# Performance work log

Hardware: AMD Instinct MI355X
Metric: run time of the kernel (lower is better)

## Reference

```python
import jax, jax.numpy as jnp
import numpy as np

B, T_Q, T_KV, D = 4, 2048, 4096, 1024
H = 16
HD = D // H  # head_dim = 64
EPS_LN = 1e-5
EPS_NORM = 1e-12


def setup_inputs() -> dict:
    key = jax.random.key(0)
    ks = jax.random.split(key, 12)
    inp = {
        'query': jax.random.normal(ks[0], (B, T_Q, D), jnp.float32),
        'key':   jax.random.normal(ks[1], (B, T_KV, D), jnp.float32),
        'value': jax.random.normal(ks[2], (B, T_KV, D), jnp.float32),
        # projections (nn.Linear stores weight as [out, in]; y = x @ W.T)
        'Wq': jax.random.normal(ks[3], (D, D), jnp.float32) * 0.02,
        'Wk': jax.random.normal(ks[4], (D, D), jnp.float32) * 0.02,
        'Wv': jax.random.normal(ks[5], (D, D), jnp.float32) * 0.02,
        'Wo': jax.random.normal(ks[6], (D, D), jnp.float32) * 0.01,
        'bo': jnp.zeros((D,), jnp.float32),
        'Wbeta':  jax.random.normal(ks[7], (H, D), jnp.float32) * 0.02,
        'bbeta':  jnp.zeros((H,), jnp.float32),
        'Walpha': jax.random.normal(ks[8], (H, D), jnp.float32) * 0.02,
        'balpha': jnp.full((H,), -1.0, jnp.float32),
        # per-head-dim LayerNorms
        'gq': jnp.ones((HD,), jnp.float32),
        'bq': jnp.zeros((HD,), jnp.float32),
        'gk': jnp.ones((HD,), jnp.float32),
        'bk': jnp.zeros((HD,), jnp.float32),
    }
    return inp


def _layernorm(x, g, b):
    mu = jnp.mean(x, axis=-1, keepdims=True)
    var = jnp.mean(jnp.square(x - mu), axis=-1, keepdims=True)
    return (x - mu) * jax.lax.rsqrt(var + EPS_LN) * g + b


def reference(query, key, value, Wq, Wk, Wv, Wo, bo,
              Wbeta, bbeta, Walpha, balpha, gq, bq, gk, bk):
    Bq, Tq, Dm = query.shape
    Tkv = key.shape[1]

    q = (query @ Wq.T).reshape(Bq, Tq, H, HD)
    k = (key   @ Wk.T).reshape(Bq, Tkv, H, HD)
    v = (value @ Wv.T).reshape(Bq, Tkv, H, HD)

    q = _layernorm(q, gq, bq)
    k = _layernorm(k, gk, bk)
    # F.normalize(k, dim=-1)
    k = k / jnp.maximum(jnp.linalg.norm(k, axis=-1, keepdims=True), EPS_NORM)

    beta  = jax.nn.sigmoid(key @ Wbeta.T  + bbeta)   # [B, Tkv, H]
    alpha = jax.nn.sigmoid(key @ Walpha.T + balpha)  # [B, Tkv, H]

    # time-major for scan: [Tkv, B, H, ...]
    k_t = jnp.moveaxis(k, 1, 0)
    v_t = jnp.moveaxis(v, 1, 0)
    b_t = jnp.moveaxis(beta, 1, 0)
    a_t = jnp.moveaxis(alpha, 1, 0)

    M0 = jnp.zeros((Bq, H, HD, HD), query.dtype)

    def step(M, inputs):
        kt, vt, bt, at = inputs  # [B,H,d],[B,H,d],[B,H],[B,H]
        Mk = jnp.einsum('bhij,bhj->bhi', M, kt)
        erase = at[..., None, None] * jnp.einsum('bhi,bhj->bhij', Mk, kt)
        write = bt[..., None, None] * jnp.einsum('bhi,bhj->bhij', vt, kt)
        return M - erase + write, None

    M, _ = jax.lax.scan(step, M0, (k_t, v_t, b_t, a_t))

    # out[b,t,h,i] = sum_j M[b,h,i,j] * q[b,t,h,j]
    out = jnp.einsum('bhij,bthj->bthi', M, q).reshape(Bq, Tq, Dm)
    out = out @ Wo.T + bo  # dropout is identity in eval mode
    return out
```

## Files before the change

kernel.cpp:

```cpp
#include <hip/hip_runtime.h>
#include <math.h>

#define TQ_LEN 2048
#define TKV_LEN 4096
#define BATCH 4
#define DMODEL 1024
#define NH 16
#define HD 64
#define NKBA 1280
#define CCH 128
#define NCHUNK (TKV_LEN / CCH)

typedef unsigned short u16;
typedef __attribute__((ext_vector_type(8))) short bf16x8;
typedef __attribute__((ext_vector_type(4))) float f32x4;

__device__ __forceinline__ u16 f2bf(float x) {
  union { float f; unsigned u; } c; c.f = x;
  unsigned r = c.u + 0x7fffu + ((c.u >> 16) & 1u);
  return (u16)(r >> 16);
}
__device__ __forceinline__ float bf2f(u16 x) {
  union { unsigned u; float f; } c; c.u = ((unsigned)x) << 16;
  return c.f;
}

__device__ __forceinline__ float wave_sum64(float x) {
#pragma unroll
  for (int off = 32; off; off >>= 1) x += __shfl_xor(x, off, 64);
  return x;
}

__global__ __launch_bounds__(256) void cvt_bf16_kernel(
    const float* __restrict__ s, u16* __restrict__ d) {
  size_t i = ((size_t)blockIdx.x * 256 + threadIdx.x) * 8;
  float4 a = *(const float4*)&s[i];
  float4 b = *(const float4*)&s[i + 4];
  union { u16 h[8]; uint4 v; } o;
  o.h[0] = f2bf(a.x); o.h[1] = f2bf(a.y); o.h[2] = f2bf(a.z); o.h[3] = f2bf(a.w);
  o.h[4] = f2bf(b.x); o.h[5] = f2bf(b.y); o.h[6] = f2bf(b.z); o.h[7] = f2bf(b.w);
  *(uint4*)&d[i] = o.v;
}

__global__ __launch_bounds__(256) void wcat_bf_kernel(
    const float* __restrict__ Wk, const float* __restrict__ Wb,
    const float* __restrict__ Wa, u16* __restrict__ Wcat) {
  int i = blockIdx.x * 256 + threadIdx.x;
  int row = i / DMODEL, col = i % DMODEL;
  float v;
  if (row < 1024)      v = Wk[i];
  else if (row < 1040) v = Wb[(row - 1024) * DMODEL + col];
  else if (row < 1056) v = Wa[(row - 1040) * DMODEL + col];
  else                 v = 0.f;
  Wcat[i] = f2bf(v);
}

#define BAR() __builtin_amdgcn_s_barrier()
#define PRIO(x) __builtin_amdgcn_s_setprio(x)
#define VMCNT(n)                                              \
  do {                                                        \
    __builtin_amdgcn_sched_barrier(0);                        \
    asm volatile("s_waitcnt vmcnt(" #n ")" ::: "memory");     \
  } while (0)

__device__ __forceinline__ void stage_half256(
    const u16* __restrict__ G, int ldg, int row0, int kc, int h,
    u16* ldsmat, int wid, int lane) {
#pragma unroll
  for (int e = 0; e < 2; ++e) {
    int j0 = wid * 64 + e * 512;
    int j = j0 + lane;
    int r = h * 128 + (j >> 3);
    int cg = (j & 7) * 8;
    const u16* g = G + (size_t)(row0 + r) * ldg + kc + cg;
    __builtin_amdgcn_global_load_lds(
        (const __attribute__((address_space(1))) void*)g,
        (__attribute__((address_space(3))) void*)(ldsmat + h * 8192 + j0 * 8),
        16, 0, 0);
  }
}

#define READ_A(L, h_)                                                         \
  do {                                                                        \
    _Pragma("unroll") for (int mf = 0; mf < 4; ++mf)                          \
    _Pragma("unroll") for (int kk = 0; kk < 2; ++kk)                          \
      af[mf][kk] = *(const bf16x8*)&(L)[(wm * 128 + (h_) * 64 + mf * 16 +     \
                                         lrow) * 64 + kk * 32 + lk8];         \
  } while (0)

#define READ_B(L, n_, dst)                                                    \
  do {                                                                        \
    _Pragma("unroll") for (int nf = 0; nf < 2; ++nf)                          \
    _Pragma("unroll") for (int kk = 0; kk < 2; ++kk)                          \
      dst[nf][kk] = *(const bf16x8*)&(L)[(wn * 64 + (n_) * 32 + nf * 16 +     \
                                          lrow) * 64 + kk * 32 + lk8];        \
  } while (0)

#define MFMA_Q(h_, n_, bfx)                                                   \
  do {                                                                        \
    _Pragma("unroll") for (int mf = 0; mf < 4; ++mf)                          \
    _Pragma("unroll") for (int nf = 0; nf < 2; ++nf)                          \
    _Pragma("unroll") for (int kk = 0; kk < 2; ++kk)                          \
      acc[h_][mf][n_][nf] = __builtin_amdgcn_mfma_f32_16x16x32_bf16(          \
          af[mf][kk], bfx[nf][kk], acc[h_][mf][n_][nf], 0, 0, 0);             \
  } while (0)

template <bool HAS_BIAS, bool OUT_BF16>
__global__ __launch_bounds__(512, 2) void gemm_bt_256(
    const u16* __restrict__ A, const u16* __restrict__ B,
    const float* __restrict__ bias, void* __restrict__ Cv,
    int K, int ldc, int nbx) {
  __shared__ u16 lds[2][2][16384];
  const int tid = threadIdx.x;
  const int lane = tid & 63, wid = tid >> 6;
  const int wm = wid >> 2, wn = wid & 3;
  const int nwg = gridDim.x, cpx = nwg >> 3, orig = blockIdx.x;
  const int swz = (orig & 7) * cpx + (orig >> 3);
  const int bm = (swz / nbx) * 256, bn = (swz % nbx) * 256;
  const int lrow = lane & 15, lk8 = (lane >> 4) * 8;
  const int NT = K >> 6;

  f32x4 acc[2][4][2][2] = {};
  bf16x8 af[4][2], bf0[2][2], bf1[2][2];

  u16* lA0 = &lds[0][0][0]; u16* lB0 = &lds[0][1][0];
  u16* lA1 = &lds[1][0][0]; u16* lB1 = &lds[1][1][0];

  stage_half256(A, K, bm, 0, 0, lA0, wid, lane);
  stage_half256(A, K, bm, 0, 1, lA0, wid, lane);
  stage_half256(B, K, bn, 0, 0, lB0, wid, lane);
  stage_half256(B, K, bn, 0, 1, lB0, wid, lane);
  stage_half256(B, K, bn, 64, 0, lB1, wid, lane);
  stage_half256(B, K, bn, 64, 1, lB1, wid, lane);
  VMCNT(0);
  BAR();

  for (int i = 0; i < NT / 2; ++i) {
    const int t0 = 2 * i, t1 = 2 * i + 1;
    READ_A(lA0, 0);
    READ_B(lB0, 0, bf0);
    stage_half256(A, K, bm, t1 * 64, 0, lA1, wid, lane);
    BAR(); PRIO(1); MFMA_Q(0, 0, bf0); PRIO(0); BAR();
    READ_B(lB0, 1, bf1);
    stage_half256(A, K, bm, t1 * 64, 1, lA1, wid, lane);
    BAR(); PRIO(1); MFMA_Q(0, 1, bf1); PRIO(0); BAR();
    READ_A(lA0, 1);
    if (t0 + 2 < NT) stage_half256(B, K, bn, (t0 + 2) * 64, 0, lB0, wid, lane);
    BAR(); PRIO(1); MFMA_Q(1, 0, bf0); PRIO(0); BAR();
    if (t0 + 2 < NT) stage_half256(B, K, bn, (t0 + 2) * 64, 1, lB0, wid, lane);
    BAR(); PRIO(1); MFMA_Q(1, 1, bf1); PRIO(0);
    VMCNT(4);
    BAR();
    READ_A(lA1, 0);
    READ_B(lB1, 0, bf0);
    if (t0 + 2 < NT) stage_half256(A, K, bm, (t0 + 2) * 64, 0, lA0, wid, lane);
    BAR(); PRIO(1); MFMA_Q(0, 0, bf0); PRIO(0); BAR();
    READ_B(lB1, 1, bf1);
    if (t0 + 2 < NT) stage_half256(A, K, bm, (t0 + 2) * 64, 1, lA0, wid, lane);
    BAR(); PRIO(1); MFMA_Q(0, 1, bf1); PRIO(0); BAR();
    READ_A(lA1, 1);
    if (t1 + 2 < NT) stage_half256(B, K, bn, (t1 + 2) * 64, 0, lB1, wid, lane);
    BAR(); PRIO(1); MFMA_Q(1, 0, bf0); PRIO(0); BAR();
    if (t1 + 2 < NT) stage_half256(B, K, bn, (t1 + 2) * 64, 1, lB1, wid, lane);
    BAR(); PRIO(1); MFMA_Q(1, 1, bf1); PRIO(0);
    VMCNT(4);
    BAR();
  }

#pragma unroll
  for (int h = 0; h < 2; ++h)
#pragma unroll
    for (int n = 0; n < 2; ++n)
#pragma unroll
      for (int mf = 0; mf < 4; ++mf)
#pragma unroll
        for (int nf = 0; nf < 2; ++nf) {
          int col = bn + wn * 64 + n * 32 + nf * 16 + (lane & 15);
          float bv = HAS_BIAS ? bias[col] : 0.f;
          int row0 = bm + wm * 128 + h * 64 + mf * 16 + (lane >> 4) * 4;
#pragma unroll
          for (int ii = 0; ii < 4; ++ii) {
            float vout = acc[h][mf][n][nf][ii] + bv;
            if (OUT_BF16)
              ((u16*)Cv)[(size_t)(row0 + ii) * ldc + col] = f2bf(vout);
            else
              ((float*)Cv)[(size_t)(row0 + ii) * ldc + col] = vout;
          }
        }
}

__global__ __launch_bounds__(256) void ln_q_kernel(float* __restrict__ q,
                                                   const float* __restrict__ g,
                                                   const float* __restrict__ b) {
  int gidx = blockIdx.x * 4 + (threadIdx.x >> 6);
  int lane = threadIdx.x & 63;
  int row = gidx >> 4, h = gidx & 15;
  float* p = q + (size_t)row * DMODEL + h * HD + lane;
  float x = *p;
  float mu = wave_sum64(x) * (1.f / 64.f);
  float d = x - mu;
  float var = wave_sum64(d * d) * (1.f / 64.f);
  float y = d * rsqrtf(var + 1e-5f) * g[lane] + b[lane];
  *p = y;
}

__global__ __launch_bounds__(256) void ln_k_kernel(float* __restrict__ kb,
                                                   const float* __restrict__ g,
                                                   const float* __restrict__ b) {
  int gidx = blockIdx.x * 4 + (threadIdx.x >> 6);
  int lane = threadIdx.x & 63;
  int row = gidx >> 4, h = gidx & 15;
  float* p = kb + (size_t)row * NKBA + h * HD + lane;
  float x = *p;
  float mu = wave_sum64(x) * (1.f / 64.f);
  float d = x - mu;
  float var = wave_sum64(d * d) * (1.f / 64.f);
  float y = d * rsqrtf(var + 1e-5f) * g[lane] + b[lane];
  float s2 = wave_sum64(y * y);
  y = y / fmaxf(sqrtf(s2), 1e-12f);
  *p = y;
}

__global__ __launch_bounds__(256) void sig_kernel(
    const float* __restrict__ kb, const float* __restrict__ bb,
    const float* __restrict__ ba, float* __restrict__ beta,
    float* __restrict__ alpha) {
  int i = blockIdx.x * 256 + threadIdx.x;
  int row = i >> 4, h = i & 15;
  float lb = kb[(size_t)row * NKBA + 1024 + h] + bb[h];
  float la = kb[(size_t)row * NKBA + 1040 + h] + ba[h];
  beta[i]  = 1.f / (1.f + expf(-lb));
  alpha[i] = 1.f / (1.f + expf(-la));
}

__global__ __launch_bounds__(64, 2) void chunk_scan_kernel(
    const float* __restrict__ kb, const u16* __restrict__ v,
    const float* __restrict__ beta, const float* __restrict__ alpha,
    float* __restrict__ Pbuf, float* __restrict__ Sbuf) {
  __shared__ float klds[2][64];
  int slot = blockIdx.x;
  int bh = slot / NCHUNK, ck = slot % NCHUNK;
  int b = bh >> 4, h = bh & 15;
  int lane = threadIdx.x;
  int t0 = ck * CCH;
  const float* kbase = kb + ((size_t)b * TKV_LEN + t0) * NKBA + h * HD;
  const u16* vbase = v + ((size_t)b * TKV_LEN + t0) * DMODEL + h * HD;
  const float* bbase = beta + ((size_t)b * TKV_LEN + t0) * NH + h;
  const float* abase = alpha + ((size_t)b * TKV_LEN + t0) * NH + h;

  float P[64], S[64];
#pragma unroll
  for (int j = 0; j < 64; ++j) { P[j] = (j == lane) ? 1.f : 0.f; S[j] = 0.f; }

  klds[0][lane] = kbase[lane];
  float kn = kbase[(size_t)NKBA + lane];
  float vn = bf2f(vbase[lane]);
  float btn = bbase[0];
  float atn = abase[0];

  for (int t = 0; t < CCH; ++t) {
    float vc = vn, bt = btn, at = atn;
    if (t + 1 < CCH) {
      vn = bf2f(vbase[(size_t)(t + 1) * DMODEL + lane]);
      btn = bbase[(size_t)(t + 1) * NH];
      atn = abase[(size_t)(t + 1) * NH];
    }
    klds[(t + 1) & 1][lane] = kn;
    kn = (t + 2 < CCH) ? kbase[(size_t)(t + 2) * NKBA + lane] : 0.f;
    const float* kcur = klds[t & 1];
    float pk0 = 0.f, pk1 = 0.f, sk0 = 0.f, sk1 = 0.f;
#pragma unroll
    for (int g = 0; g < 4; ++g) {
      float4 ka = *(const float4*)&kcur[g * 16 + 0];
      float4 kc = *(const float4*)&kcur[g * 16 + 4];
      float4 ke = *(const float4*)&kcur[g * 16 + 8];
      float4 kg = *(const float4*)&kcur[g * 16 + 12];
      pk0 = fmaf(P[g*16+ 0], ka.x, pk0); pk1 = fmaf(P[g*16+ 1], ka.y, pk1);
      pk0 = fmaf(P[g*16+ 2], ka.z, pk0); pk1 = fmaf(P[g*16+ 3], ka.w, pk1);
      pk0 = fmaf(P[g*16+ 4], kc.x, pk0); pk1 = fmaf(P[g*16+ 5], kc.y, pk1);
      pk0 = fmaf(P[g*16+ 6], kc.z, pk0); pk1 = fmaf(P[g*16+ 7], kc.w, pk1);
      pk0 = fmaf(P[g*16+ 8], ke.x, pk0); pk1 = fmaf(P[g*16+ 9], ke.y, pk1);
      pk0 = fmaf(P[g*16+10], ke.z, pk0); pk1 = fmaf(P[g*16+11], ke.w, pk1);
      pk0 = fmaf(P[g*16+12], kg.x, pk0); pk1 = fmaf(P[g*16+13], kg.y, pk1);
      pk0 = fmaf(P[g*16+14], kg.z, pk0); pk1 = fmaf(P[g*16+15], kg.w, pk1);
      sk0 = fmaf(S[g*16+ 0], ka.x, sk0); sk1 = fmaf(S[g*16+ 1], ka.y, sk1);
      sk0 = fmaf(S[g*16+ 2], ka.z, sk0); sk1 = fmaf(S[g*16+ 3], ka.w, sk1);
      sk0 = fmaf(S[g*16+ 4], kc.x, sk0); sk1 = fmaf(S[g*16+ 5], kc.y, sk1);
      sk0 = fmaf(S[g*16+ 6], kc.z, sk0); sk1 = fmaf(S[g*16+ 7], kc.w, sk1);
      sk0 = fmaf(S[g*16+ 8], ke.x, sk0); sk1 = fmaf(S[g*16+ 9], ke.y, sk1);
      sk0 = fmaf(S[g*16+10], ke.z, sk0); sk1 = fmaf(S[g*16+11], ke.w, sk1);
      sk0 = fmaf(S[g*16+12], kg.x, sk0); sk1 = fmaf(S[g*16+13], kg.y, sk1);
      sk0 = fmaf(S[g*16+14], kg.z, sk0); sk1 = fmaf(S[g*16+15], kg.w, sk1);
    }
    float cp = -at * (pk0 + pk1);
    float cs = fmaf(bt, vc, -at * (sk0 + sk1));
#pragma unroll
    for (int g = 0; g < 4; ++g) {
      float4 ka = *(const float4*)&kcur[g * 16 + 0];
      float4 kc = *(const float4*)&kcur[g * 16 + 4];
      float4 ke = *(const float4*)&kcur[g * 16 + 8];
      float4 kg = *(const float4*)&kcur[g * 16 + 12];
      P[g*16+ 0] = fmaf(cp, ka.x, P[g*16+ 0]); P[g*16+ 1] = fmaf(cp, ka.y, P[g*16+ 1]);
      P[g*16+ 2] = fmaf(cp, ka.z, P[g*16+ 2]); P[g*16+ 3] = fmaf(cp, ka.w, P[g*16+ 3]);
      P[g*16+ 4] = fmaf(cp, kc.x, P[g*16+ 4]); P[g*16+ 5] = fmaf(cp, kc.y, P[g*16+ 5]);
      P[g*16+ 6] = fmaf(cp, kc.z, P[g*16+ 6]); P[g*16+ 7] = fmaf(cp, kc.w, P[g*16+ 7]);
      P[g*16+ 8] = fmaf(cp, ke.x, P[g*16+ 8]); P[g*16+ 9] = fmaf(cp, ke.y, P[g*16+ 9]);
      P[g*16+10] = fmaf(cp, ke.z, P[g*16+10]); P[g*16+11] = fmaf(cp, ke.w, P[g*16+11]);
      P[g*16+12] = fmaf(cp, kg.x, P[g*16+12]); P[g*16+13] = fmaf(cp, kg.y, P[g*16+13]);
      P[g*16+14] = fmaf(cp, kg.z, P[g*16+14]); P[g*16+15] = fmaf(cp, kg.w, P[g*16+15]);
      S[g*16+ 0] = fmaf(cs, ka.x, S[g*16+ 0]); S[g*16+ 1] = fmaf(cs, ka.y, S[g*16+ 1]);
      S[g*16+ 2] = fmaf(cs, ka.z, S[g*16+ 2]); S[g*16+ 3] = fmaf(cs, ka.w, S[g*16+ 3]);
      S[g*16+ 4] = fmaf(cs, kc.x, S[g*16+ 4]); S[g*16+ 5] = fmaf(cs, kc.y, S[g*16+ 5]);
      S[g*16+ 6] = fmaf(cs, kc.z, S[g*16+ 6]); S[g*16+ 7] = fmaf(cs, kc.w, S[g*16+ 7]);
      S[g*16+ 8] = fmaf(cs, ke.x, S[g*16+ 8]); S[g*16+ 9] = fmaf(cs, ke.y, S[g*16+ 9]);
      S[g*16+10] = fmaf(cs, ke.z, S[g*16+10]); S[g*16+11] = fmaf(cs, ke.w, S[g*16+11]);
      S[g*16+12] = fmaf(cs, kg.x, S[g*16+12]); S[g*16+13] = fmaf(cs, kg.y, S[g*16+13]);
      S[g*16+14] = fmaf(cs, kg.z, S[g*16+14]); S[g*16+15] = fmaf(cs, kg.w, S[g*16+15]);
    }
  }
  float* po = Pbuf + (size_t)slot * 4096 + (size_t)lane * 64;
  float* so = Sbuf + (size_t)slot * 4096 + (size_t)lane * 64;
#pragma unroll
  for (int j4 = 0; j4 < 16; ++j4) {
    *(float4*)&po[j4 * 4] = make_float4(P[4 * j4], P[4 * j4 + 1], P[4 * j4 + 2], P[4 * j4 + 3]);
    *(float4*)&so[j4 * 4] = make_float4(S[4 * j4], S[4 * j4 + 1], S[4 * j4 + 2], S[4 * j4 + 3]);
  }
}

__global__ __launch_bounds__(256) void fold_kernel(
    const float* __restrict__ Pin, const float* __restrict__ Sin,
    float* __restrict__ Pout, float* __restrict__ Sout, int nitems) {
  __shared__ float Pa[64][68], Sa[64][68], Pc[64][68], Sc[64][68];
  const int tid = threadIdx.x;
  const int r0 = (tid >> 4) * 4, c0 = (tid & 15) * 4;
  for (int l = tid; l < 4096; l += 256) {
    int r = l >> 6, c = l & 63;
    Pa[r][c] = (r == c) ? 1.f : 0.f;
    Sa[r][c] = 0.f;
  }
  for (int item = 0; item < nitems; ++item) {
    const float* pg = Pin + ((size_t)blockIdx.x * nitems + item) * 4096;
    const float* sg = Sin + ((size_t)blockIdx.x * nitems + item) * 4096;
#pragma unroll
    for (int e = 0; e < 4; ++e) {
      int l = tid * 16 + e * 4;
      int r = l >> 6, c = l & 63;
      *(float4*)&Pc[r][c] = *(const float4*)&pg[l];
      *(float4*)&Sc[r][c] = *(const float4*)&sg[l];
    }
    __syncthreads();
    float accP[4][4] = {}, accS[4][4] = {};
#pragma unroll 4
    for (int j4 = 0; j4 < 16; ++j4) {
      float bmat[4][4];
#pragma unroll
      for (int jj = 0; jj < 4; ++jj) {
        float4 t = *(const float4*)&Pc[j4 * 4 + jj][c0];
        bmat[jj][0] = t.x; bmat[jj][1] = t.y; bmat[jj][2] = t.z; bmat[jj][3] = t.w;
      }
#pragma unroll
      for (int rr = 0; rr < 4; ++rr) {
        float4 tp = *(const float4*)&Pa[r0 + rr][j4 * 4];
        float4 ts = *(const float4*)&Sa[r0 + rr][j4 * 4];
        float ap[4] = {tp.x, tp.y, tp.z, tp.w};
        float as[4] = {ts.x, ts.y, ts.z, ts.w};
#pragma unroll
        for (int jj = 0; jj < 4; ++jj)
#pragma unroll
          for (int cc = 0; cc < 4; ++cc) {
            accP[rr][cc] = fmaf(ap[jj], bmat[jj][cc], accP[rr][cc]);
            accS[rr][cc] = fmaf(as[jj], bmat[jj][cc], accS[rr][cc]);
          }
      }
    }
#pragma unroll
    for (int rr = 0; rr < 4; ++rr)
#pragma unroll
      for (int cc = 0; cc < 4; ++cc) accS[rr][cc] += Sc[r0 + rr][c0 + cc];
    __syncthreads();
#pragma unroll
    for (int rr = 0; rr < 4; ++rr)
#pragma unroll
      for (int cc = 0; cc < 4; ++cc) {
        Pa[r0 + rr][c0 + cc] = accP[rr][cc];
        Sa[r0 + rr][c0 + cc] = accS[rr][cc];
      }
  }
  __syncthreads();
  float* po = Pout + (size_t)blockIdx.x * 4096;
  float* so = Sout + (size_t)blockIdx.x * 4096;
#pragma unroll
  for (int e = 0; e < 4; ++e) {
    int l = tid * 16 + e * 4;
    int r = l >> 6, c = l & 63;
    *(float4*)&po[l] = *(const float4*)&Pa[r][c];
    *(float4*)&so[l] = *(const float4*)&Sa[r][c];
  }
}

__global__ __launch_bounds__(256) void outm_kernel(
    const float* __restrict__ Mg, const float* __restrict__ q,
    u16* __restrict__ attn) {
  __shared__ float Ml[64][65];
  int bh = blockIdx.x;
  int tchunk = blockIdx.y;
  int b = bh >> 4, h = bh & 15;
  int tid = threadIdx.x;
  const float* mg = Mg + (size_t)bh * 4096;
#pragma unroll
  for (int e = 0; e < 16; ++e) {
    int l = tid + e * 256;
    Ml[l >> 6][l & 63] = mg[l];
  }
  __syncthreads();
  int lane = tid & 63, tt = tid >> 6;
  const float* qb = q + ((size_t)b * TQ_LEN + tchunk * 256) * DMODEL + h * HD;
  u16* ob = attn + ((size_t)b * TQ_LEN + tchunk * 256) * DMODEL + h * HD;
  for (int it = 0; it < 64; ++it) {
    int t = it * 4 + tt;
    const float* qr = qb + (size_t)t * DMODEL;
    float acc = 0.f;
#pragma unroll
    for (int j4 = 0; j4 < 16; ++j4) {
      float4 qv = *(const float4*)&qr[j4 * 4];
      acc += Ml[lane][j4 * 4 + 0] * qv.x + Ml[lane][j4 * 4 + 1] * qv.y +
             Ml[lane][j4 * 4 + 2] * qv.z + Ml[lane][j4 * 4 + 3] * qv.w;
    }
    ob[(size_t)t * DMODEL + lane] = f2bf(acc);
  }
}

extern "C" void kernel_launch(void* const* d_in, const int* in_sizes, int n_in,
                              void* d_out, int out_size, void* d_ws,
                              size_t ws_size, hipStream_t stream) {
  const float* query = (const float*)d_in[0];
  const float* key   = (const float*)d_in[1];
  const float* value = (const float*)d_in[2];
  const float* Wq    = (const float*)d_in[3];
  const float* Wk    = (const float*)d_in[4];
  const float* Wv    = (const float*)d_in[5];
  const float* Wo    = (const float*)d_in[6];
  const float* bo    = (const float*)d_in[7];
  const float* Wbeta = (const float*)d_in[8];
  const float* bbeta = (const float*)d_in[9];
  const float* Walpha= (const float*)d_in[10];
  const float* balpha= (const float*)d_in[11];
  const float* gq    = (const float*)d_in[12];
  const float* bq    = (const float*)d_in[13];
  const float* gk    = (const float*)d_in[14];
  const float* bk    = (const float*)d_in[15];
  float* out = (float*)d_out;

  const int MQ = BATCH * TQ_LEN;
  const int MKV = BATCH * TKV_LEN;
  const int NSLOT = 64 * NCHUNK;

  float* ws = (float*)d_ws;
  size_t off = 0;
  u16* Wcat_bf = (u16*)(ws + off); off += (size_t)NKBA * DMODEL / 2;
  u16* Wq_bf   = (u16*)(ws + off); off += (size_t)DMODEL * DMODEL / 2;
  u16* Wv_bf   = (u16*)(ws + off); off += (size_t)DMODEL * DMODEL / 2;
  u16* Wo_bf   = (u16*)(ws + off); off += (size_t)DMODEL * DMODEL / 2;
  u16* qbf = (u16*)(ws + off); size_t qbf_f = off; off += (size_t)MQ * DMODEL / 2;
  u16* kbf = (u16*)(ws + off); size_t kbf_f = off; off += (size_t)MKV * DMODEL / 2;
  u16* vbf = (u16*)(ws + off); size_t vbf_f = off; off += (size_t)MKV * DMODEL / 2;
  float* qp   = ws + off; off += (size_t)MQ * DMODEL;
  float* kba  = ws + off; size_t kba_f = off; off += (size_t)MKV * NKBA;
  u16* vpb = (u16*)(ws + off); off += (size_t)MKV * DMODEL / 2;
  float* Pbuf = ws + kbf_f;
  float* Sbuf = ws + vbf_f;
  float* Gp   = ws + qbf_f;
  float* Gs   = ws + qbf_f + 1048576;
  float* Fp   = ws + qbf_f + 2097152;
  float* beta = ws + qbf_f + 2359296;
  float* alpha= ws + qbf_f + 2621440;
  float* Mg   = ws + qbf_f + 2883584;
  u16* attn_bf = (u16*)(ws + kba_f);

  wcat_bf_kernel<<<NKBA * DMODEL / 256, 256, 0, stream>>>(Wk, Wbeta, Walpha, Wcat_bf);
  cvt_bf16_kernel<<<DMODEL * DMODEL / 2048, 256, 0, stream>>>(Wq, Wq_bf);
  cvt_bf16_kernel<<<DMODEL * DMODEL / 2048, 256, 0, stream>>>(Wv, Wv_bf);
  cvt_bf16_kernel<<<DMODEL * DMODEL / 2048, 256, 0, stream>>>(Wo, Wo_bf);
  cvt_bf16_kernel<<<MQ * DMODEL / 2048, 256, 0, stream>>>(query, qbf);
  cvt_bf16_kernel<<<MKV * DMODEL / 2048, 256, 0, stream>>>(key, kbf);
  cvt_bf16_kernel<<<MKV * DMODEL / 2048, 256, 0, stream>>>(value, vbf);
  gemm_bt_256<false, false><<<(DMODEL / 256) * (MQ / 256), 512, 0, stream>>>(
      qbf, Wq_bf, nullptr, qp, DMODEL, DMODEL, DMODEL / 256);
  gemm_bt_256<false, false><<<(NKBA / 256) * (MKV / 256), 512, 0, stream>>>(
      kbf, Wcat_bf, nullptr, kba, DMODEL, NKBA, NKBA / 256);
  gemm_bt_256<false, true><<<(DMODEL / 256) * (MKV / 256), 512, 0, stream>>>(
      vbf, Wv_bf, nullptr, vpb, DMODEL, DMODEL, DMODEL / 256);
  ln_q_kernel<<<MQ * NH / 4, 256, 0, stream>>>(qp, gq, bq);
  ln_k_kernel<<<MKV * NH / 4, 256, 0, stream>>>(kba, gk, bk);
  sig_kernel<<<MKV * NH / 256, 256, 0, stream>>>(kba, bbeta, balpha, beta, alpha);
  chunk_scan_kernel<<<NSLOT, 64, 0, stream>>>(kba, vpb, beta, alpha, Pbuf, Sbuf);
  fold_kernel<<<NSLOT / 8, 256, 0, stream>>>(Pbuf, Sbuf, Gp, Gs, 8);
  fold_kernel<<<64, 256, 0, stream>>>(Gp, Gs, Fp, Mg, 4);
  outm_kernel<<<dim3(64, TQ_LEN / 256), 256, 0, stream>>>(Mg, qp, attn_bf);
  gemm_bt_256<true, false><<<(DMODEL / 256) * (MQ / 256), 512, 0, stream>>>(
      attn_bf, Wo_bf, bo, out, DMODEL, DMODEL, DMODEL / 256);
  (void)in_sizes; (void)n_in; (void)out_size; (void)ws_size;
}
```

Baseline: 632.9 us.

## Shrink GEMM tiles to 128x256 with XOR-swizzled LDS and restructured pipeline

Replaces the 256x256 bf16 GEMM tile with a 128x256 tile. This halves the accumulator registers and doubles the workgroup count, so more of the CUs are filled for these matrix sizes. It adds an XOR swizzle on the LDS column groups to avoid bank conflicts on the MFMA fragment reads. The load/compute schedule is rewritten with new vmcnt/lgkmcnt waits and barriers. The trade-off is less data reuse per tile (more global traffic for B) and a more intricate wait schedule that could stall or race.

```diff
diff --git a/kernel.cpp b/kernel.cpp
--- a/kernel.cpp
+++ b/kernel.cpp
@@ -62,30 +62,35 @@
     __builtin_amdgcn_sched_barrier(0);                        \
     asm volatile("s_waitcnt vmcnt(" #n ")" ::: "memory");     \
   } while (0)
-
-__device__ __forceinline__ void stage_half256(
-    const u16* __restrict__ G, int ldg, int row0, int kc, int h,
-    u16* ldsmat, int wid, int lane) {
+#define LGKM0()                                               \
+  do {                                                        \
+    asm volatile("s_waitcnt lgkmcnt(0)" ::: "memory");        \
+    __builtin_amdgcn_sched_barrier(0);                        \
+  } while (0)
+
+__device__ __forceinline__ void stage128(
+    const u16* __restrict__ G, int ldg, int row0, int kc,
+    u16* ldsbase, int wid, int lane) {
 #pragma unroll
   for (int e = 0; e < 2; ++e) {
     int j0 = wid * 64 + e * 512;
     int j = j0 + lane;
-    int r = h * 128 + (j >> 3);
-    int cg = (j & 7) * 8;
+    int r = j >> 3;
+    int cg = ((j & 7) ^ (r & 7)) * 8;
     const u16* g = G + (size_t)(row0 + r) * ldg + kc + cg;
     __builtin_amdgcn_global_load_lds(
         (const __attribute__((address_space(1))) void*)g,
-        (__attribute__((address_space(3))) void*)(ldsmat + h * 8192 + j0 * 8),
+        (__attribute__((address_space(3))) void*)(ldsbase + (size_t)j0 * 8),
         16, 0, 0);
   }
 }
 
-#define READ_A(L, h_)                                                         \
+#define READ_A(L)                                                             \
   do {                                                                        \
     _Pragma("unroll") for (int mf = 0; mf < 4; ++mf)                          \
     _Pragma("unroll") for (int kk = 0; kk < 2; ++kk)                          \
-      af[mf][kk] = *(const bf16x8*)&(L)[(wm * 128 + (h_) * 64 + mf * 16 +     \
-                                         lrow) * 64 + kk * 32 + lk8];         \
+      af[mf][kk] = *(const bf16x8*)&(L)[(wm * 64 + mf * 16 + lrow) * 64 +     \
+                                        (((kk * 4 + (lane >> 4)) ^ xorg) * 8)];\
   } while (0)
 
 #define READ_B(L, n_, dst)                                                    \
@@ -93,100 +98,98 @@
     _Pragma("unroll") for (int nf = 0; nf < 2; ++nf)                          \
     _Pragma("unroll") for (int kk = 0; kk < 2; ++kk)                          \
       dst[nf][kk] = *(const bf16x8*)&(L)[(wn * 64 + (n_) * 32 + nf * 16 +     \
-                                          lrow) * 64 + kk * 32 + lk8];        \
+                                          lrow) * 64 +                        \
+                                         (((kk * 4 + (lane >> 4)) ^ xorg) * 8)];\
   } while (0)
 
-#define MFMA_Q(h_, n_, bfx)                                                   \
+#define MFMA_Q(n_, bfx)                                                       \
   do {                                                                        \
     _Pragma("unroll") for (int mf = 0; mf < 4; ++mf)                          \
     _Pragma("unroll") for (int nf = 0; nf < 2; ++nf)                          \
     _Pragma("unroll") for (int kk = 0; kk < 2; ++kk)                          \
-      acc[h_][mf][n_][nf] = __builtin_amdgcn_mfma_f32_16x16x32_bf16(          \
-          af[mf][kk], bfx[nf][kk], acc[h_][mf][n_][nf], 0, 0, 0);             \
+      acc[mf][n_][nf] = __builtin_amdgcn_mfma_f32_16x16x32_bf16(              \
+          af[mf][kk], bfx[nf][kk], acc[mf][n_][nf], 0, 0, 0);                 \
   } while (0)
 
 template <bool HAS_BIAS, bool OUT_BF16>
-__global__ __launch_bounds__(512, 2) void gemm_bt_256(
+__global__ __launch_bounds__(512, 2) void gemm_bt_128x256(
     const u16* __restrict__ A, const u16* __restrict__ B,
     const float* __restrict__ bias, void* __restrict__ Cv,
     int K, int ldc, int nbx) {
-  __shared__ u16 lds[2][2][16384];
+  __shared__ u16 lA[2][8192];
+  __shared__ u16 lB[2][16384];
   const int tid = threadIdx.x;
   const int lane = tid & 63, wid = tid >> 6;
   const int wm = wid >> 2, wn = wid & 3;
   const int nwg = gridDim.x, cpx = nwg >> 3, orig = blockIdx.x;
   const int swz = (orig & 7) * cpx + (orig >> 3);
-  const int bm = (swz / nbx) * 256, bn = (swz % nbx) * 256;
-  const int lrow = lane & 15, lk8 = (lane >> 4) * 8;
+  const int bm = (swz / nbx) * 128, bn = (swz % nbx) * 256;
+  const int lrow = lane & 15;
+  const int xorg = lrow & 7;
   const int NT = K >> 6;
 
-  f32x4 acc[2][4][2][2] = {};
+  f32x4 acc[4][2][2] = {};
   bf16x8 af[4][2], bf0[2][2], bf1[2][2];
 
-  u16* lA0 = &lds[0][0][0]; u16* lB0 = &lds[0][1][0];
-  u16* lA1 = &lds[1][0][0]; u16* lB1 = &lds[1][1][0];
-
-  stage_half256(A, K, bm, 0, 0, lA0, wid, lane);
-  stage_half256(A, K, bm, 0, 1, lA0, wid, lane);
-  stage_half256(B, K, bn, 0, 0, lB0, wid, lane);
-  stage_half256(B, K, bn, 0, 1, lB0, wid, lane);
-  stage_half256(B, K, bn, 64, 0, lB1, wid, lane);
-  stage_half256(B, K, bn, 64, 1, lB1, wid, lane);
+  u16* lA0 = &lA[0][0]; u16* lA1 = &lA[1][0];
+  u16* lB0 = &lB[0][0]; u16* lB1 = &lB[1][0];
+
+  stage128(A, K, bm, 0, lA0, wid, lane);
+  stage128(B, K, bn, 0, lB0, wid, lane);
+  stage128(B, K, bn + 128, 0, lB0 + 8192, wid, lane);
+  stage128(A, K, bm, 64, lA1, wid, lane);
+  stage128(B, K, bn, 64, lB1, wid, lane);
+  stage128(B, K, bn + 128, 64, lB1 + 8192, wid, lane);
   VMCNT(0);
   BAR();
 
   for (int i = 0; i < NT / 2; ++i) {
-    const int t0 = 2 * i, t1 = 2 * i + 1;
-    READ_A(lA0, 0);
+    const int t0 = 2 * i;
+    const bool more = (t0 + 2) < NT;
+    READ_A(lA0);
     READ_B(lB0, 0, bf0);
-    stage_half256(A, K, bm, t1 * 64, 0, lA1, wid, lane);
-    BAR(); PRIO(1); MFMA_Q(0, 0, bf0); PRIO(0); BAR();
     READ_B(lB0, 1, bf1);
-    stage_half256(A, K, bm, t1 * 64, 1, lA1, wid, lane);
-    BAR(); PRIO(1); MFMA_Q(0, 1, bf1); PRIO(0); BAR();
-    READ_A(lA0, 1);
-    if (t0 + 2 < NT) stage_half256(B, K, bn, (t0 + 2) * 64, 0, lB0, wid, lane);
-    BAR(); PRIO(1); MFMA_Q(1, 0, bf0); PRIO(0); BAR();
-    if (t0 + 2 < NT) stage_half256(B, K, bn, (t0 + 2) * 64, 1, lB0, wid, lane);
-    BAR(); PRIO(1); MFMA_Q(1, 1, bf1); PRIO(0);
-    VMCNT(4);
+    BAR(); PRIO(1); MFMA_Q(0, bf0); PRIO(0); BAR();
+    if (more) stage128(A, K, bm, (t0 + 2) * 64, lA0, wid, lane);
+    BAR(); PRIO(1); MFMA_Q(1, bf1); PRIO(0);
+    if (more) { VMCNT(2); } else { VMCNT(0); }
     BAR();
-    READ_A(lA1, 0);
+    READ_A(lA1);
     READ_B(lB1, 0, bf0);
-    if (t0 + 2 < NT) stage_half256(A, K, bm, (t0 + 2) * 64, 0, lA0, wid, lane);
-    BAR(); PRIO(1); MFMA_Q(0, 0, bf0); PRIO(0); BAR();
     READ_B(lB1, 1, bf1);
-    if (t0 + 2 < NT) stage_half256(A, K, bm, (t0 + 2) * 64, 1, lA0, wid, lane);
-    BAR(); PRIO(1); MFMA_Q(0, 1, bf1); PRIO(0); BAR();
-    READ_A(lA1, 1);
-    if (t1 + 2 < NT) stage_half256(B, K, bn, (t1 + 2) * 64, 0, lB1, wid, lane);
-    BAR(); PRIO(1); MFMA_Q(1, 0, bf0); PRIO(0); BAR();
-    if (t1 + 2 < NT) stage_half256(B, K, bn, (t1 + 2) * 64, 1, lB1, wid, lane);
-    BAR(); PRIO(1); MFMA_Q(1, 1, bf1); PRIO(0);
-    VMCNT(4);
+    if (more) stage128(B, K, bn, (t0 + 2) * 64, lB0, wid, lane);
+    BAR(); PRIO(1); MFMA_Q(0, bf0); PRIO(0);
+    LGKM0();
     BAR();
-  }
-
-#pragma unroll
-  for (int h = 0; h < 2; ++h)
-#pragma unroll
-    for (int n = 0; n < 2; ++n)
-#pragma unroll
-      for (int mf = 0; mf < 4; ++mf)
-#pragma unroll
-        for (int nf = 0; nf < 2; ++nf) {
-          int col = bn + wn * 64 + n * 32 + nf * 16 + (lane & 15);
-          float bv = HAS_BIAS ? bias[col] : 0.f;
-          int row0 = bm + wm * 128 + h * 64 + mf * 16 + (lane >> 4) * 4;
-#pragma unroll
-          for (int ii = 0; ii < 4; ++ii) {
-            float vout = acc[h][mf][n][nf][ii] + bv;
-            if (OUT_BF16)
-              ((u16*)Cv)[(size_t)(row0 + ii) * ldc + col] = f2bf(vout);
-            else
-              ((float*)Cv)[(size_t)(row0 + ii) * ldc + col] = vout;
-          }
+    if (more) {
+      stage128(B, K, bn + 128, (t0 + 2) * 64, lB0 + 8192, wid, lane);
+      stage128(A, K, bm, (t0 + 3) * 64, lA1, wid, lane);
+      stage128(B, K, bn, (t0 + 3) * 64, lB1, wid, lane);
+      stage128(B, K, bn + 128, (t0 + 3) * 64, lB1 + 8192, wid, lane);
+    }
+    BAR(); PRIO(1); MFMA_Q(1, bf1); PRIO(0);
+    VMCNT(6);
+    BAR();
+  }
+
+#pragma unroll
+  for (int n = 0; n < 2; ++n)
+#pragma unroll
+    for (int mf = 0; mf < 4; ++mf)
+#pragma unroll
+      for (int nf = 0; nf < 2; ++nf) {
+        int col = bn + wn * 64 + n * 32 + nf * 16 + (lane & 15);
+        float bv = HAS_BIAS ? bias[col] : 0.f;
+        int row0 = bm + wm * 64 + mf * 16 + (lane >> 4) * 4;
+#pragma unroll
+        for (int ii = 0; ii < 4; ++ii) {
+          float vout = acc[mf][n][nf][ii] + bv;
+          if (OUT_BF16)
+            ((u16*)Cv)[(size_t)(row0 + ii) * ldc + col] = f2bf(vout);
+          else
+            ((float*)Cv)[(size_t)(row0 + ii) * ldc + col] = vout;
         }
+      }
 }
 
 __global__ __launch_bounds__(256) void ln_q_kernel(float* __restrict__ q,
@@ -484,11 +487,11 @@
   cvt_bf16_kernel<<<MQ * DMODEL / 2048, 256, 0, stream>>>(query, qbf);
   cvt_bf16_kernel<<<MKV * DMODEL / 2048, 256, 0, stream>>>(key, kbf);
   cvt_bf16_kernel<<<MKV * DMODEL / 2048, 256, 0, stream>>>(value, vbf);
-  gemm_bt_256<false, false><<<(DMODEL / 256) * (MQ / 256), 512, 0, stream>>>(
+  gemm_bt_128x256<false, false><<<(DMODEL / 256) * (MQ / 128), 512, 0, stream>>>(
       qbf, Wq_bf, nullptr, qp, DMODEL, DMODEL, DMODEL / 256);
-  gemm_bt_256<false, false><<<(NKBA / 256) * (MKV / 256), 512, 0, stream>>>(
+  gemm_bt_128x256<false, false><<<(NKBA / 256) * (MKV / 128), 512, 0, stream>>>(
       kbf, Wcat_bf, nullptr, kba, DMODEL, NKBA, NKBA / 256);
-  gemm_bt_256<false, true><<<(DMODEL / 256) * (MKV / 256), 512, 0, stream>>>(
+  gemm_bt_128x256<false, true><<<(DMODEL / 256) * (MKV / 128), 512, 0, stream>>>(
       vbf, Wv_bf, nullptr, vpb, DMODEL, DMODEL, DMODEL / 256);
   ln_q_kernel<<<MQ * NH / 4, 256, 0, stream>>>(qp, gq, bq);
   ln_k_kernel<<<MKV * NH / 4, 256, 0, stream>>>(kba, gk, bk);
@@ -497,7 +500,7 @@
   fold_kernel<<<NSLOT / 8, 256, 0, stream>>>(Pbuf, Sbuf, Gp, Gs, 8);
   fold_kernel<<<64, 256, 0, stream>>>(Gp, Gs, Fp, Mg, 4);
   outm_kernel<<<dim3(64, TQ_LEN / 256), 256, 0, stream>>>(Mg, qp, attn_bf);
-  gemm_bt_256<true, false><<<(DMODEL / 256) * (MQ / 256), 512, 0, stream>>>(
+  gemm_bt_128x256<true, false><<<(DMODEL / 256) * (MQ / 128), 512, 0, stream>>>(
       attn_bf, Wo_bf, bo, out, DMODEL, DMODEL, DMODEL / 256);
   (void)in_sizes; (void)n_in; (void)out_size; (void)ws_size;
 }
```

Result: faster. 588.3 us (-7.1%).
